# Performance work log

Hardware: AMD Instinct MI355X
Metric: run time of the kernel (lower is better)

The kernel has to match this reference:

```python
import jax, jax.numpy as jnp
import numpy as np

B, T, TWO_H = 64, 512, 1024  # batch, prev decoding steps, 2*hidden_dim


def setup_inputs() -> dict:
    key = jax.random.key(0)
    k1, k2, k3 = jax.random.split(key, 3)
    h_d_t = jax.random.normal(k1, (B, TWO_H), dtype=jnp.float32)
    prev_h_dec = jax.random.normal(k2, (B, T, TWO_H), dtype=jnp.float32)
    # nn.Bilinear(2H, 2H, attn_dim=1) weight, trunc_norm_init_std ~ 1e-4 typical
    W = jax.random.normal(k3, (1, TWO_H, TWO_H), dtype=jnp.float32) * 1e-4
    return {"h_d_t": h_d_t, "prev_h_dec": prev_h_dec, "W": W}


def reference(h_d_t, prev_h_dec, W):
    # Bilinear score: s[b,t] = h_d_t[b] @ W[0] @ prev_h_dec[b,t]
    q = jnp.einsum('bd,de->be', h_d_t, W[0])          # (B, 2H) -- one small GEMM
    attn_score = jnp.einsum('be,bte->bt', q, prev_h_dec)  # (B, T)
    alpha_t = jax.nn.softmax(attn_score, axis=1)      # (B, T)
    ct_d = jnp.einsum('bt,btd->bd', alpha_t, prev_h_dec)  # (B, 2H)
    new_prev = jnp.concatenate([prev_h_dec, h_d_t[:, None, :]], axis=1)  # (B, T+1, 2H)
    return (ct_d, new_prev)
```

## Files before the change

### kernel.cpp

```cpp
#include <hip/hip_runtime.h>
#include <math.h>

#define BB    64
#define TT    512
#define TWOH  1024
#define RPW   4
#define WPB   4
#define TC    (RPW * WPB)
#define NCHUNK (TT / TC)
#define KSPLIT 4
#define NP_STRIDE ((TT + 1) * TWOH)

typedef float vfloat4 __attribute__((ext_vector_type(4)));


__global__ __launch_bounds__(256) void k_qgemm(const float* __restrict__ h,
                                               const float* __restrict__ W,
                                               float* __restrict__ qpart) {
    const int tid = threadIdx.x;
    const int e   = blockIdx.x * 256 + tid;
    const int b   = blockIdx.y;
    const int k   = blockIdx.z;
    const int d0  = k * (TWOH / KSPLIT);

    __shared__ float sh[TWOH / KSPLIT];
    sh[tid] = h[b * TWOH + d0 + tid];
    __syncthreads();

    const float* __restrict__ Wp = W + (size_t)d0 * TWOH + e;
    float acc = 0.f;
    #pragma unroll 16
    for (int d = 0; d < TWOH / KSPLIT; ++d)
        acc = fmaf(sh[d], Wp[(size_t)d * TWOH], acc);

    qpart[((size_t)k * BB + b) * TWOH + e] = acc;
}

__global__ __launch_bounds__(256, 4) void k_scores_ct(const float* __restrict__ prev,
                                                      const float* __restrict__ qpart,
                                                      float* __restrict__ out_np,
                                                      float* __restrict__ ws_m,
                                                      float* __restrict__ ws_l,
                                                      float* __restrict__ ws_ct) {
    const int tid  = threadIdx.x;
    const int lane = tid & 63;
    const int wid  = tid >> 6;
    const int c    = blockIdx.x;
    const int b    = blockIdx.y;
    const int t0   = c * TC + wid * RPW;

    __shared__ float s_ct[WPB][TWOH];
    __shared__ float s_m[WPB];
    __shared__ float s_l[WPB];

    const vfloat4* __restrict__ qp = (const vfloat4*)qpart;
    vfloat4 q[4];
    #pragma unroll
    for (int j = 0; j < 4; ++j)
        q[j] = qp[(0 * BB + b) * 256 + j * 64 + lane]
             + qp[(1 * BB + b) * 256 + j * 64 + lane]
             + qp[(2 * BB + b) * 256 + j * 64 + lane]
             + qp[(3 * BB + b) * 256 + j * 64 + lane];

    const vfloat4* __restrict__ prow =
        (const vfloat4*)(prev + ((size_t)b * TT + (size_t)t0) * TWOH) + lane;
    vfloat4* __restrict__ nprow =
        (vfloat4*)(out_np + (size_t)b * NP_STRIDE + (size_t)t0 * TWOH) + lane;

    vfloat4 cv[RPW][4];
    #pragma unroll
    for (int r = 0; r < RPW; ++r)
        #pragma unroll
        for (int j = 0; j < 4; ++j)
            cv[r][j] = prow[r * 256 + j * 64];

    #pragma unroll
    for (int r = 0; r < RPW; ++r)
        #pragma unroll
        for (int j = 0; j < 4; ++j)
            nprow[r * 256 + j * 64] = cv[r][j];

    float pd[RPW];
    #pragma unroll
    for (int r = 0; r < RPW; ++r) {
        float d0 = cv[r][0].x * q[0].x;
        d0 = fmaf(cv[r][0].y, q[0].y, d0);
        d0 = fmaf(cv[r][0].z, q[0].z, d0);
        d0 = fmaf(cv[r][0].w, q[0].w, d0);
        float d1 = cv[r][1].x * q[1].x;
        d1 = fmaf(cv[r][1].y, q[1].y, d1);
        d1 = fmaf(cv[r][1].z, q[1].z, d1);
        d1 = fmaf(cv[r][1].w, q[1].w, d1);
        float d2 = cv[r][2].x * q[2].x;
        d2 = fmaf(cv[r][2].y, q[2].y, d2);
        d2 = fmaf(cv[r][2].z, q[2].z, d2);
        d2 = fmaf(cv[r][2].w, q[2].w, d2);
        float d3 = cv[r][3].x * q[3].x;
        d3 = fmaf(cv[r][3].y, q[3].y, d3);
        d3 = fmaf(cv[r][3].z, q[3].z, d3);
        d3 = fmaf(cv[r][3].w, q[3].w, d3);
        pd[r] = (d0 + d1) + (d2 + d3);
    }
    #pragma unroll
    for (int r = 0; r < RPW; ++r)
        #pragma unroll
        for (int off = 32; off > 0; off >>= 1)
            pd[r] += __shfl_xor(pd[r], off, 64);

    const float m = fmaxf(fmaxf(pd[0], pd[1]), fmaxf(pd[2], pd[3]));
    float a[RPW];
    float l = 0.f;
    #pragma unroll
    for (int r = 0; r < RPW; ++r) {
        a[r] = __expf(pd[r] - m);
        l += a[r];
    }
    vfloat4 ct[4];
    #pragma unroll
    for (int j = 0; j < 4; ++j) ct[j] = (vfloat4)(0.f);
    #pragma unroll
    for (int r = 0; r < RPW; ++r)
        #pragma unroll
        for (int j = 0; j < 4; ++j) {
            ct[j].x = fmaf(a[r], cv[r][j].x, ct[j].x);
            ct[j].y = fmaf(a[r], cv[r][j].y, ct[j].y);
            ct[j].z = fmaf(a[r], cv[r][j].z, ct[j].z);
            ct[j].w = fmaf(a[r], cv[r][j].w, ct[j].w);
        }

    vfloat4* __restrict__ sct = (vfloat4*)&s_ct[wid][0];
    #pragma unroll
    for (int j = 0; j < 4; ++j) sct[j * 64 + lane] = ct[j];
    if (lane == 0) { s_m[wid] = m; s_l[wid] = l; }
    __syncthreads();

    const float M = fmaxf(fmaxf(s_m[0], s_m[1]), fmaxf(s_m[2], s_m[3]));
    float L = 0.f;
    float co[WPB];
    #pragma unroll
    for (int w = 0; w < WPB; ++w) {
        co[w] = __expf(s_m[w] - M);
        L = fmaf(co[w], s_l[w], L);
    }
    vfloat4 o = (vfloat4)(0.f);
    #pragma unroll
    for (int w = 0; w < WPB; ++w) {
        const vfloat4 v = ((const vfloat4*)&s_ct[w][0])[tid];
        o.x = fmaf(co[w], v.x, o.x);
        o.y = fmaf(co[w], v.y, o.y);
        o.z = fmaf(co[w], v.z, o.z);
        o.w = fmaf(co[w], v.w, o.w);
    }
    ((vfloat4*)(ws_ct + ((size_t)b * NCHUNK + c) * TWOH))[tid] = o;
    if (tid == 0) {
        ws_m[b * NCHUNK + c] = M;
        ws_l[b * NCHUNK + c] = L;
    }
}

__global__ __launch_bounds__(256) void k_finalize(const float* __restrict__ h,
                                                  const float* __restrict__ ws_m,
                                                  const float* __restrict__ ws_l,
                                                  const float* __restrict__ ws_ct,
                                                  float* __restrict__ out_ct,
                                                  float* __restrict__ out_np) {
    const int tid = threadIdx.x;
    const int e   = blockIdx.x * 256 + tid;
    const int b   = blockIdx.y;

    const float* __restrict__ wm = ws_m + b * NCHUNK;
    const float* __restrict__ wl = ws_l + b * NCHUNK;

    float M = -INFINITY;
    #pragma unroll
    for (int i = 0; i < NCHUNK; ++i) M = fmaxf(M, wm[i]);

    const float* __restrict__ cp = ws_ct + (size_t)b * NCHUNK * TWOH + e;
    float L = 0.f;
    float acc = 0.f;
    #pragma unroll
    for (int i = 0; i < NCHUNK; ++i) {
        const float ce = __expf(wm[i] - M);
        L   = fmaf(ce, wl[i], L);
        acc = fmaf(ce, cp[(size_t)i * TWOH], acc);
    }
    out_ct[b * TWOH + e] = acc * (1.0f / L);

    out_np[(size_t)b * NP_STRIDE + (size_t)TT * TWOH + e] = h[b * TWOH + e];
}

extern "C" void kernel_launch(void* const* d_in, const int* in_sizes, int n_in,
                              void* d_out, int out_size, void* d_ws, size_t ws_size,
                              hipStream_t stream) {
    const float* h    = (const float*)d_in[0];
    const float* prev = (const float*)d_in[1];
    const float* W    = (const float*)d_in[2];
    float* out    = (float*)d_out;
    float* out_ct = out;
    float* out_np = out + BB * TWOH;

    float* qpart = (float*)d_ws;
    float* wsm   = qpart + KSPLIT * BB * TWOH;
    float* wsl   = wsm + BB * NCHUNK;
    float* wsc   = wsl + BB * NCHUNK;

    k_qgemm<<<dim3(4, BB, KSPLIT), 256, 0, stream>>>(h, W, qpart);
    k_scores_ct<<<dim3(NCHUNK, BB), 256, 0, stream>>>(prev, qpart, out_np, wsm, wsl, wsc);
    k_finalize<<<dim3(4, BB), 256, 0, stream>>>(h, wsm, wsl, wsc, out_ct, out_np);
}
```

Baseline: 262.1 us.

## Stage prev rows into LDS via direct global-to-LDS loads and halve rows per wave

Rows of prev_h_dec are now loaded straight into shared memory with 16-byte global_load_lds, instead of being held in registers as 16 vfloat4 per thread. They are then read from LDS for the copy-out, the dot products and the weighted context sum. Rows per wave drop from 4 to 2, which doubles the number of chunk blocks, and the per-wave context partials reuse the same LDS buffer. This aims to cut register pressure and raise memory-level parallelism. In exchange there is extra LDS traffic, twice the workspace partials, and a longer reduction loop in the finalize kernel.

```diff
diff --git a/kernel.cpp b/kernel.cpp
--- a/kernel.cpp
+++ b/kernel.cpp
@@ -4,15 +4,22 @@
 #define BB    64
 #define TT    512
 #define TWOH  1024
-#define RPW   4
+#define RPW   2
 #define WPB   4
-#define TC    (RPW * WPB)
-#define NCHUNK (TT / TC)
+#define TCB   (RPW * WPB)
+#define NCHUNK (TT / TCB)
 #define KSPLIT 4
 #define NP_STRIDE ((TT + 1) * TWOH)
 
 typedef float vfloat4 __attribute__((ext_vector_type(4)));
 
+
+__device__ __forceinline__ void gload_lds16(const float* g, float* l) {
+    __builtin_amdgcn_global_load_lds(
+        (const __attribute__((address_space(1))) unsigned int*)g,
+        (__attribute__((address_space(3))) unsigned int*)l,
+        16, 0, 0);
+}
 
 __global__ __launch_bounds__(256) void k_qgemm(const float* __restrict__ h,
                                                const float* __restrict__ W,
@@ -47,11 +54,16 @@
     const int wid  = tid >> 6;
     const int c    = blockIdx.x;
     const int b    = blockIdx.y;
-    const int t0   = c * TC + wid * RPW;
-
-    __shared__ float s_ct[WPB][TWOH];
-    __shared__ float s_m[WPB];
-    __shared__ float s_l[WPB];
+    const int t0   = c * TCB + wid * RPW;
+
+    __shared__ float smem[WPB][RPW][TWOH];
+
+    const float* gbase = prev + ((size_t)b * TT + t0) * TWOH;
+    #pragma unroll
+    for (int r = 0; r < RPW; ++r)
+        #pragma unroll
+        for (int j = 0; j < 4; ++j)
+            gload_lds16(gbase + r * TWOH + j * 256 + lane * 4, &smem[wid][r][j * 256]);
 
     const vfloat4* __restrict__ qp = (const vfloat4*)qpart;
     vfloat4 q[4];
@@ -62,43 +74,31 @@
              + qp[(2 * BB + b) * 256 + j * 64 + lane]
              + qp[(3 * BB + b) * 256 + j * 64 + lane];
 
-    const vfloat4* __restrict__ prow =
-        (const vfloat4*)(prev + ((size_t)b * TT + (size_t)t0) * TWOH) + lane;
+    asm volatile("s_waitcnt vmcnt(0)" ::: "memory");
+    __builtin_amdgcn_sched_barrier(0);
+
+    const vfloat4* srow = (const vfloat4*)&smem[wid][0][0];
     vfloat4* __restrict__ nprow =
         (vfloat4*)(out_np + (size_t)b * NP_STRIDE + (size_t)t0 * TWOH) + lane;
-
-    vfloat4 cv[RPW][4];
-    #pragma unroll
-    for (int r = 0; r < RPW; ++r)
-        #pragma unroll
-        for (int j = 0; j < 4; ++j)
-            cv[r][j] = prow[r * 256 + j * 64];
-
-    #pragma unroll
-    for (int r = 0; r < RPW; ++r)
-        #pragma unroll
-        for (int j = 0; j < 4; ++j)
-            nprow[r * 256 + j * 64] = cv[r][j];
-
     float pd[RPW];
     #pragma unroll
     for (int r = 0; r < RPW; ++r) {
-        float d0 = cv[r][0].x * q[0].x;
-        d0 = fmaf(cv[r][0].y, q[0].y, d0);
-        d0 = fmaf(cv[r][0].z, q[0].z, d0);
-        d0 = fmaf(cv[r][0].w, q[0].w, d0);
-        float d1 = cv[r][1].x * q[1].x;
-        d1 = fmaf(cv[r][1].y, q[1].y, d1);
-        d1 = fmaf(cv[r][1].z, q[1].z, d1);
-        d1 = fmaf(cv[r][1].w, q[1].w, d1);
-        float d2 = cv[r][2].x * q[2].x;
-        d2 = fmaf(cv[r][2].y, q[2].y, d2);
-        d2 = fmaf(cv[r][2].z, q[2].z, d2);
-        d2 = fmaf(cv[r][2].w, q[2].w, d2);
-        float d3 = cv[r][3].x * q[3].x;
-        d3 = fmaf(cv[r][3].y, q[3].y, d3);
-        d3 = fmaf(cv[r][3].z, q[3].z, d3);
-        d3 = fmaf(cv[r][3].w, q[3].w, d3);
+        const vfloat4 v0 = srow[r * 256 +       lane];
+        const vfloat4 v1 = srow[r * 256 +  64 + lane];
+        const vfloat4 v2 = srow[r * 256 + 128 + lane];
+        const vfloat4 v3 = srow[r * 256 + 192 + lane];
+        nprow[r * 256      ] = v0;
+        nprow[r * 256 +  64] = v1;
+        nprow[r * 256 + 128] = v2;
+        nprow[r * 256 + 192] = v3;
+        float d0 = v0.x * q[0].x; d0 = fmaf(v0.y, q[0].y, d0);
+        d0 = fmaf(v0.z, q[0].z, d0); d0 = fmaf(v0.w, q[0].w, d0);
+        float d1 = v1.x * q[1].x; d1 = fmaf(v1.y, q[1].y, d1);
+        d1 = fmaf(v1.z, q[1].z, d1); d1 = fmaf(v1.w, q[1].w, d1);
+        float d2 = v2.x * q[2].x; d2 = fmaf(v2.y, q[2].y, d2);
+        d2 = fmaf(v2.z, q[2].z, d2); d2 = fmaf(v2.w, q[2].w, d2);
+        float d3 = v3.x * q[3].x; d3 = fmaf(v3.y, q[3].y, d3);
+        d3 = fmaf(v3.z, q[3].z, d3); d3 = fmaf(v3.w, q[3].w, d3);
         pd[r] = (d0 + d1) + (d2 + d3);
     }
     #pragma unroll
@@ -107,49 +107,52 @@
         for (int off = 32; off > 0; off >>= 1)
             pd[r] += __shfl_xor(pd[r], off, 64);
 
-    const float m = fmaxf(fmaxf(pd[0], pd[1]), fmaxf(pd[2], pd[3]));
+    const float m = fmaxf(pd[0], pd[1]);
     float a[RPW];
     float l = 0.f;
     #pragma unroll
+    for (int r = 0; r < RPW; ++r) { a[r] = __expf(pd[r] - m); l += a[r]; }
+
+    vfloat4 ct[4];
+    #pragma unroll
+    for (int j = 0; j < 4; ++j) ct[j] = (vfloat4)(0.f);
+    #pragma unroll
     for (int r = 0; r < RPW; ++r) {
-        a[r] = __expf(pd[r] - m);
-        l += a[r];
-    }
-    vfloat4 ct[4];
-    #pragma unroll
-    for (int j = 0; j < 4; ++j) ct[j] = (vfloat4)(0.f);
-    #pragma unroll
-    for (int r = 0; r < RPW; ++r)
         #pragma unroll
         for (int j = 0; j < 4; ++j) {
-            ct[j].x = fmaf(a[r], cv[r][j].x, ct[j].x);
-            ct[j].y = fmaf(a[r], cv[r][j].y, ct[j].y);
-            ct[j].z = fmaf(a[r], cv[r][j].z, ct[j].z);
-            ct[j].w = fmaf(a[r], cv[r][j].w, ct[j].w);
+            const vfloat4 v = srow[r * 256 + j * 64 + lane];
+            ct[j].x = fmaf(a[r], v.x, ct[j].x);
+            ct[j].y = fmaf(a[r], v.y, ct[j].y);
+            ct[j].z = fmaf(a[r], v.z, ct[j].z);
+            ct[j].w = fmaf(a[r], v.w, ct[j].w);
         }
-
-    vfloat4* __restrict__ sct = (vfloat4*)&s_ct[wid][0];
-    #pragma unroll
-    for (int j = 0; j < 4; ++j) sct[j * 64 + lane] = ct[j];
-    if (lane == 0) { s_m[wid] = m; s_l[wid] = l; }
+    }
+
+    float* cb = &smem[wid][0][0];
+    #pragma unroll
+    for (int j = 0; j < 4; ++j) ((vfloat4*)cb)[j * 64 + lane] = ct[j];
+    if (lane == 0) { cb[TWOH] = m; cb[TWOH + 1] = l; }
     __syncthreads();
 
-    const float M = fmaxf(fmaxf(s_m[0], s_m[1]), fmaxf(s_m[2], s_m[3]));
+    const float* s0 = &smem[0][0][0];
+    float mw[WPB], lw[WPB];
+    #pragma unroll
+    for (int w = 0; w < WPB; ++w) {
+        mw[w] = s0[w * (RPW * TWOH) + TWOH];
+        lw[w] = s0[w * (RPW * TWOH) + TWOH + 1];
+    }
+    const float M = fmaxf(fmaxf(mw[0], mw[1]), fmaxf(mw[2], mw[3]));
     float L = 0.f;
-    float co[WPB];
+    vfloat4 o = (vfloat4)(0.f);
     #pragma unroll
     for (int w = 0; w < WPB; ++w) {
-        co[w] = __expf(s_m[w] - M);
-        L = fmaf(co[w], s_l[w], L);
-    }
-    vfloat4 o = (vfloat4)(0.f);
-    #pragma unroll
-    for (int w = 0; w < WPB; ++w) {
-        const vfloat4 v = ((const vfloat4*)&s_ct[w][0])[tid];
-        o.x = fmaf(co[w], v.x, o.x);
-        o.y = fmaf(co[w], v.y, o.y);
-        o.z = fmaf(co[w], v.z, o.z);
-        o.w = fmaf(co[w], v.w, o.w);
+        const float co = __expf(mw[w] - M);
+        L = fmaf(co, lw[w], L);
+        const vfloat4 v = ((const vfloat4*)(s0 + w * (RPW * TWOH)))[tid];
+        o.x = fmaf(co, v.x, o.x);
+        o.y = fmaf(co, v.y, o.y);
+        o.z = fmaf(co, v.z, o.z);
+        o.w = fmaf(co, v.w, o.w);
     }
     ((vfloat4*)(ws_ct + ((size_t)b * NCHUNK + c) * TWOH))[tid] = o;
     if (tid == 0) {
```

Result: no change. 264.8 us (+1.0%).
